# Kernel optimization log

Measured on AMD Instinct MI355X. Metric: run time of the kernel, lower is better.

Reference implementation:

```python
import jax, jax.numpy as jnp
import numpy as np
import math

B, LQ, LK = 4, 1024, 2048
QD, KD, VD = 768, 512, 512
H, NH = 1024, 16
HD = H // NH

def setup_inputs() -> dict:
    key = jax.random.key(0)
    ks = jax.random.split(key, 11)
    s = 0.02
    return {
        "query": jax.random.normal(ks[0], (B, LQ, QD), jnp.float32),
        "key": jax.random.normal(ks[1], (B, LK, KD), jnp.float32),
        "value": jax.random.normal(ks[2], (B, LK, VD), jnp.float32),
        "Wq": jax.random.normal(ks[3], (QD, H), jnp.float32) * s,
        "bq": jnp.zeros((H,), jnp.float32),
        "Wk": jax.random.normal(ks[4], (KD, H), jnp.float32) * s,
        "bk": jnp.zeros((H,), jnp.float32),
        "Wv": jax.random.normal(ks[5], (VD, H), jnp.float32) * s,
        "bv": jnp.zeros((H,), jnp.float32),
        "Wo": jax.random.normal(ks[6], (H, H), jnp.float32) * s,
        "bo": jnp.zeros((H,), jnp.float32),
    }

def reference(query, key, value, Wq, bq, Wk, bk, Wv, bv, Wo, bo):
    # project and split heads: [B, L, H] -> [B, NH, L, HD]
    def heads(x):
        b, l, _ = x.shape
        return x.reshape(b, l, NH, HD).transpose(0, 2, 1, 3)
    q = heads(query @ Wq + bq)   # [B, NH, LQ, HD]
    k = heads(key @ Wk + bk)     # [B, NH, LK, HD]
    v = heads(value @ Wv + bv)   # [B, NH, LK, HD]
    scores = jnp.einsum('bhqd,bhkd->bhqk', q, k) / math.sqrt(HD)
    weights = jax.nn.softmax(scores, axis=-1)  # dropout inactive (eval / rate used deterministically as identity)
    att = jnp.einsum('bhqk,bhkd->bhqd', weights, v)
    att = att.transpose(0, 2, 1, 3).reshape(query.shape[0], -1, H)
    out = att @ Wo + bo
    return out
```

## Files before the change

### kernel.cpp

```cpp
#include <hip/hip_runtime.h>
#include <math.h>

using bf16x8 = __attribute__((ext_vector_type(8))) short;
using f32x4  = __attribute__((ext_vector_type(4))) float;

namespace {
constexpr int kB  = 4;
constexpr int kLQ = 1024;
constexpr int kLK = 2048;
constexpr int kH  = 1024;
constexpr int kHD = 64;
}

__device__ __forceinline__ unsigned short f2bf(float x) {
  union { float f; unsigned int u; } v; v.f = x;
  unsigned int r = v.u + 0x7fffu + ((v.u >> 16) & 1u);
  return (unsigned short)(r >> 16);
}

typedef const __attribute__((address_space(1))) unsigned int guint_t;
typedef __attribute__((address_space(3))) unsigned int luint_t;
__device__ __forceinline__ void g2l16(const void* g, void* l) {
  __builtin_amdgcn_global_load_lds(
      (guint_t*)g,
      (luint_t*)(unsigned int)(unsigned long long)l,
      16, 0, 0);
}

__global__ __launch_bounds__(256) void prep_kernel(
    const float* __restrict__ q, const float* __restrict__ k,
    const float* __restrict__ v, const float* __restrict__ Wq,
    const float* __restrict__ Wk, const float* __restrict__ Wv,
    const float* __restrict__ Wo, unsigned short* __restrict__ qo,
    unsigned short* __restrict__ ko, unsigned short* __restrict__ vo,
    unsigned short* __restrict__ WqT, unsigned short* __restrict__ WkT,
    unsigned short* __restrict__ WvT, unsigned short* __restrict__ WoT)
{
  __shared__ float tile[64][65];
  const int t = threadIdx.x;
  if (blockIdx.x < 5632) {
    int c = blockIdx.x * 256 + t;
    const float* src; unsigned short* dst;
    if (c < 393216)      { src = q; dst = qo; }
    else if (c < 917504) { src = k; dst = ko; c -= 393216; }
    else                 { src = v; dst = vo; c -= 917504; }
    const int i = c * 8;
    const float4 a = *(const float4*)(src + i);
    const float4 b = *(const float4*)(src + i + 4);
    uint4 o;
    o.x = (unsigned int)f2bf(a.x) | ((unsigned int)f2bf(a.y) << 16);
    o.y = (unsigned int)f2bf(a.z) | ((unsigned int)f2bf(a.w) << 16);
    o.z = (unsigned int)f2bf(b.x) | ((unsigned int)f2bf(b.y) << 16);
    o.w = (unsigned int)f2bf(b.z) | ((unsigned int)f2bf(b.w) << 16);
    *(uint4*)(dst + i) = o;
    return;
  }
  int id = blockIdx.x - 5632;
  const float* W; unsigned short* Wt; int Kd;
  if (id < 192)      { W = Wq; Wt = WqT; Kd = 768; }
  else if (id < 320) { W = Wk; Wt = WkT; Kd = 512;  id -= 192; }
  else if (id < 448) { W = Wv; Wt = WvT; Kd = 512;  id -= 320; }
  else               { W = Wo; Wt = WoT; Kd = 1024; id -= 448; }
  const int Nd = 1024;
  const int n0 = (id & 15) * 64;
  const int k0 = (id >> 4) * 64;
  const int rr = t >> 4;
  const int c4 = t & 15;
#pragma unroll
  for (int i = 0; i < 4; ++i) {
    const int row = i * 16 + rr;
    const float4 vv = *(const float4*)(W + (size_t)(k0 + row) * Nd + n0 + c4 * 4);
    tile[row][c4*4+0] = vv.x; tile[row][c4*4+1] = vv.y;
    tile[row][c4*4+2] = vv.z; tile[row][c4*4+3] = vv.w;
  }
  __syncthreads();
#pragma unroll
  for (int i = 0; i < 4; ++i) {
    const int n = i * 16 + rr;
    ushort4 o;
    o.x = f2bf(tile[c4*4+0][n]); o.y = f2bf(tile[c4*4+1][n]);
    o.z = f2bf(tile[c4*4+2][n]); o.w = f2bf(tile[c4*4+3][n]);
    *(ushort4*)(Wt + (size_t)(n0 + n) * Kd + k0 + c4 * 4) = o;
  }
}

__device__ __forceinline__ void gemm_body(
    const unsigned short* __restrict__ A, const unsigned short* __restrict__ Bt,
    const float* __restrict__ bias, void* __restrict__ Cout,
    int N, int K, int bx, int by, int mode, char* lds)
{
  const int t    = threadIdx.x;
  const int lane = t & 63;
  const int w    = t >> 6;
  const int l15  = lane & 15;
  const int lq8  = (lane >> 4) * 8;
  const int lq4  = (lane >> 4) * 4;
  const int r0   = by * 128;
  const int c0   = bx * 128;
  const int wm   = w >> 1, wn = w & 1;

  f32x4 acc[4][4] = {};

#pragma unroll
  for (int i = 0; i < 4; ++i) {
    const int g = w * 4 + i;
    const unsigned short* src = (g < 8) ? A : Bt;
    const int rbase = (g < 8) ? (r0 + g * 16) : (c0 + (g - 8) * 16);
    g2l16(src + (size_t)(rbase + l15) * K + lq8, lds + g * 1024 + lane * 16);
  }

  int pb = 0;
  for (int k0 = 0; k0 < K; k0 += 32, pb ^= 1) {
    __syncthreads();
    char* buf = lds + pb * 16384;
    if (k0 + 32 < K) {
      char* nbuf = lds + (pb ^ 1) * 16384;
#pragma unroll
      for (int i = 0; i < 4; ++i) {
        const int g = w * 4 + i;
        const unsigned short* src = (g < 8) ? A : Bt;
        const int rbase = (g < 8) ? (r0 + g * 16) : (c0 + (g - 8) * 16);
        g2l16(src + (size_t)(rbase + l15) * K + k0 + 32 + lq8, nbuf + g * 1024 + lane * 16);
      }
    }
    bf16x8 af[4], bfr[4];
#pragma unroll
    for (int i = 0; i < 4; ++i) af[i]  = *(const bf16x8*)(buf + (wm*4 + i) * 1024 + lane * 16);
#pragma unroll
    for (int j = 0; j < 4; ++j) bfr[j] = *(const bf16x8*)(buf + 8192 + (wn*4 + j) * 1024 + lane * 16);
#pragma unroll
    for (int i = 0; i < 4; ++i)
#pragma unroll
      for (int j = 0; j < 4; ++j)
        acc[i][j] = __builtin_amdgcn_mfma_f32_16x16x32_bf16(af[i], bfr[j], acc[i][j], 0, 0, 0);
  }

#pragma unroll
  for (int j = 0; j < 4; ++j) {
    const int col = c0 + wn * 64 + j * 16 + l15;
    const float bcol = bias[col];
#pragma unroll
    for (int i = 0; i < 4; ++i) {
      const int row = r0 + wm * 64 + i * 16 + lq4;
      if (mode == 0) {
        float* out = (float*)Cout;
#pragma unroll
        for (int r = 0; r < 4; ++r) out[(size_t)(row + r) * N + col] = acc[i][j][r] + bcol;
      } else if (mode == 1) {
        unsigned short* out = (unsigned short*)Cout;
#pragma unroll
        for (int r = 0; r < 4; ++r) out[(size_t)(row + r) * N + col] = f2bf(acc[i][j][r] + bcol);
      } else {
        unsigned short* out = (unsigned short*)Cout;
        const int bb = row >> 11;
        const int lk = row & 2047;
        ushort4 o;
        o.x = f2bf(acc[i][j][0] + bcol); o.y = f2bf(acc[i][j][1] + bcol);
        o.z = f2bf(acc[i][j][2] + bcol); o.w = f2bf(acc[i][j][3] + bcol);
        *(ushort4*)(out + (size_t)(bb * kH + col) * kLK + lk) = o;
      }
    }
  }
}

__global__ __launch_bounds__(256) void qkv_gemm_kernel(
    const unsigned short* __restrict__ qA, const unsigned short* __restrict__ WqT,
    const float* __restrict__ bq, unsigned short* __restrict__ Qb,
    const unsigned short* __restrict__ kA, const unsigned short* __restrict__ WkT,
    const float* __restrict__ bk, unsigned short* __restrict__ Kb,
    const unsigned short* __restrict__ vA, const unsigned short* __restrict__ WvT,
    const float* __restrict__ bv, unsigned short* __restrict__ Vtw)
{
  __shared__ __align__(16) char lds[32768];
  int id = blockIdx.x;
  if (id < 256) {
    gemm_body(qA, WqT, bq, Qb, 1024, 768, id & 7, id >> 3, 1, lds);
  } else if (id < 768) {
    id -= 256;
    gemm_body(kA, WkT, bk, Kb, 1024, 512, id & 7, id >> 3, 1, lds);
  } else {
    id -= 768;
    gemm_body(vA, WvT, bv, Vtw, 1024, 512, id & 7, id >> 3, 2, lds);
  }
}

__global__ __launch_bounds__(256) void out_gemm_kernel(
    const unsigned short* __restrict__ A, const unsigned short* __restrict__ Bt,
    const float* __restrict__ bias, float* __restrict__ C)
{
  __shared__ __align__(16) char lds[32768];
  gemm_body(A, Bt, bias, C, 1024, 1024, blockIdx.x, blockIdx.y, 0, lds);
}

__global__ __launch_bounds__(256) void attn_mfma_kernel(
    const unsigned short* __restrict__ Q, const unsigned short* __restrict__ K,
    const unsigned short* __restrict__ Vt, unsigned short* __restrict__ O)
{
  __shared__ __align__(16) char lds[51200];
  constexpr int POFF = 32768;
  const int t    = threadIdx.x;
  const int lane = t & 63;
  const int w    = t >> 6;
  const int l15  = lane & 15;
  const int lq8  = (lane >> 4) * 8;
  const int lq4  = (lane >> 4) * 4;
  const int flat = blockIdx.x;
  const int bh   = flat & 63;
  const int qb   = flat >> 6;
  const int h    = bh & 15;
  const int b    = bh >> 4;
  const int q0   = qb * 128;
  const int hoff = h * kHD;

  bf16x8 qf[2][2];
#pragma unroll
  for (int qi = 0; qi < 2; ++qi)
#pragma unroll
    for (int kh = 0; kh < 2; ++kh)
      qf[qi][kh] = *(const bf16x8*)(Q + (size_t)(b*kLQ + q0 + w*32 + qi*16 + l15) * kH
                                      + hoff + kh*32 + lq8);

  f32x4 acc[2][4] = {};
  float lsum[2][4] = {};

#pragma unroll
  for (int i = 0; i < 4; ++i) {
    const int g = w * 4 + i;
    if (g < 8) {
      g2l16(K + (size_t)(b*kLK + (g >> 1)*16 + l15) * kH + hoff + (g & 1)*32 + lq8,
            lds + g * 1024 + lane * 16);
    } else {
      const int gg = g - 8;
      g2l16(Vt + (size_t)(b*kH + hoff + (gg >> 1)*16 + l15) * kLK + (gg & 1)*32 + lq8,
            lds + 8192 + gg * 1024 + lane * 16);
    }
  }

  int pb = 0;
  for (int kt = 0; kt < kLK / 64; ++kt, pb ^= 1) {
    __syncthreads();
    char* buf = lds + pb * 16384;
    if (kt + 1 < kLK / 64) {
      char* nbuf = lds + (pb ^ 1) * 16384;
      const int kc1 = (kt + 1) * 64;
#pragma unroll
      for (int i = 0; i < 4; ++i) {
        const int g = w * 4 + i;
        if (g < 8) {
          g2l16(K + (size_t)(b*kLK + kc1 + (g >> 1)*16 + l15) * kH + hoff + (g & 1)*32 + lq8,
                nbuf + g * 1024 + lane * 16);
        } else {
          const int gg = g - 8;
          g2l16(Vt + (size_t)(b*kH + hoff + (gg >> 1)*16 + l15) * kLK + kc1 + (gg & 1)*32 + lq8,
                nbuf + 8192 + gg * 1024 + lane * 16);
        }
      }
    }

    f32x4 s[2][4];
#pragma unroll
    for (int kcf = 0; kcf < 4; ++kcf) {
      const bf16x8 kf0 = *(const bf16x8*)(buf + (kcf*2 + 0) * 1024 + lane * 16);
      const bf16x8 kf1 = *(const bf16x8*)(buf + (kcf*2 + 1) * 1024 + lane * 16);
#pragma unroll
      for (int qi = 0; qi < 2; ++qi) {
        f32x4 z = {};
        z = __builtin_amdgcn_mfma_f32_16x16x32_bf16(qf[qi][0], kf0, z, 0, 0, 0);
        z = __builtin_amdgcn_mfma_f32_16x16x32_bf16(qf[qi][1], kf1, z, 0, 0, 0);
        s[qi][kcf] = z;
      }
    }

#pragma unroll
    for (int qi = 0; qi < 2; ++qi)
#pragma unroll
      for (int kcf = 0; kcf < 4; ++kcf)
#pragma unroll
        for (int r = 0; r < 4; ++r) {
          const float p = __builtin_amdgcn_exp2f(s[qi][kcf][r] * 0.18033688011112042f);
          lsum[qi][r] += p;
          union { float f; unsigned int u; } pu; pu.f = p;
          *(unsigned short*)(lds + POFF +
              ((w*32 + qi*16 + lq4 + r) * 72 + kcf*16 + l15) * 2) =
              (unsigned short)(pu.u >> 16);
        }

    bf16x8 pf[2][2];
#pragma unroll
    for (int qi = 0; qi < 2; ++qi)
#pragma unroll
      for (int kq = 0; kq < 2; ++kq)
        pf[qi][kq] = *(const bf16x8*)(lds + POFF +
            ((w*32 + qi*16 + l15) * 72 + kq*32 + lq8) * 2);
#pragma unroll
    for (int vd = 0; vd < 4; ++vd) {
      const bf16x8 vf0 = *(const bf16x8*)(buf + 8192 + (vd*2 + 0) * 1024 + lane * 16);
      const bf16x8 vf1 = *(const bf16x8*)(buf + 8192 + (vd*2 + 1) * 1024 + lane * 16);
#pragma unroll
      for (int qi = 0; qi < 2; ++qi) {
        acc[qi][vd] = __builtin_amdgcn_mfma_f32_16x16x32_bf16(pf[qi][0], vf0, acc[qi][vd], 0, 0, 0);
        acc[qi][vd] = __builtin_amdgcn_mfma_f32_16x16x32_bf16(pf[qi][1], vf1, acc[qi][vd], 0, 0, 0);
      }
    }
  }

#pragma unroll
  for (int qi = 0; qi < 2; ++qi)
#pragma unroll
    for (int r = 0; r < 4; ++r) {
      float v = lsum[qi][r];
      v += __shfl_xor(v, 1);
      v += __shfl_xor(v, 2);
      v += __shfl_xor(v, 4);
      v += __shfl_xor(v, 8);
      lsum[qi][r] = 1.f / v;
    }
#pragma unroll
  for (int qi = 0; qi < 2; ++qi)
#pragma unroll
    for (int vd = 0; vd < 4; ++vd)
#pragma unroll
      for (int r = 0; r < 4; ++r)
        O[(size_t)(b*kLQ + q0 + w*32 + qi*16 + lq4 + r) * kH + hoff + vd*16 + l15] =
            f2bf(acc[qi][vd][r] * lsum[qi][r]);
}

extern "C" void kernel_launch(void* const* d_in, const int* in_sizes, int n_in,
                              void* d_out, int out_size, void* d_ws, size_t ws_size,
                              hipStream_t stream) {
  (void)in_sizes; (void)n_in; (void)out_size; (void)ws_size;
  const float* query = (const float*)d_in[0];
  const float* key   = (const float*)d_in[1];
  const float* value = (const float*)d_in[2];
  const float* Wq = (const float*)d_in[3];
  const float* bq = (const float*)d_in[4];
  const float* Wk = (const float*)d_in[5];
  const float* bk = (const float*)d_in[6];
  const float* Wv = (const float*)d_in[7];
  const float* bv = (const float*)d_in[8];
  const float* Wo = (const float*)d_in[9];
  const float* bo = (const float*)d_in[10];
  float* out = (float*)d_out;

  unsigned short* ws  = (unsigned short*)d_ws;
  unsigned short* qA  = ws;
  unsigned short* kA  = qA  + 3145728;
  unsigned short* vA  = kA  + 4194304;
  unsigned short* WqT = vA  + 4194304;
  unsigned short* WkT = WqT + 786432;
  unsigned short* WvT = WkT + 524288;
  unsigned short* WoT = WvT + 524288;
  unsigned short* Qb  = WoT + 1048576;
  unsigned short* Kb  = Qb  + 4194304;
  unsigned short* Vtw = Kb  + 8388608;
  unsigned short* Ab  = Vtw + 8388608;

  dim3 blk(256);
  prep_kernel<<<6336, blk, 0, stream>>>(query, key, value, Wq, Wk, Wv, Wo,
                                        qA, kA, vA, WqT, WkT, WvT, WoT);
  qkv_gemm_kernel<<<1280, blk, 0, stream>>>(qA, WqT, bq, Qb,
                                            kA, WkT, bk, Kb,
                                            vA, WvT, bv, Vtw);
  attn_mfma_kernel<<<512, blk, 0, stream>>>(Qb, Kb, Vtw, Ab);
  out_gemm_kernel<<<dim3(8, 32), blk, 0, stream>>>(Ab, WoT, bo, out);
}
```

Before: 249.7 us.

## Enlarge QKV GEMM N-tile to 256 and attention query tile to 256

The QKV projection GEMM now computes 128x256 output tiles per block, with 8 B-fragments per wave and a larger double-buffered LDS area, which halves the grid and raises operand reuse per block. The attention kernel now handles 256 query rows per block (64 per wave). It double-buffers only K, loads V into a single buffer each step, and adds a barrier before the PV product. The output GEMM is inlined as its own 128x128 body. The aim is to cut redundant K/V and weight traffic, at the cost of fewer blocks (256 attention blocks), more registers per thread, and V loads no longer being prefetched a step ahead.

After: 260.8 us. 4.5% more time.

```diff
diff --git a/kernel.cpp b/kernel.cpp
--- a/kernel.cpp
+++ b/kernel.cpp
@@ -84,9 +84,9 @@
   }
 }
 
-__device__ __forceinline__ void gemm_body(
+__device__ __forceinline__ void gemm_body256(
     const unsigned short* __restrict__ A, const unsigned short* __restrict__ Bt,
-    const float* __restrict__ bias, void* __restrict__ Cout,
+    const float* __restrict__ bias, unsigned short* __restrict__ Cout,
     int N, int K, int bx, int by, int mode, char* lds)
 {
   const int t    = threadIdx.x;
@@ -96,14 +96,14 @@
   const int lq8  = (lane >> 4) * 8;
   const int lq4  = (lane >> 4) * 4;
   const int r0   = by * 128;
-  const int c0   = bx * 128;
+  const int c0   = bx * 256;
   const int wm   = w >> 1, wn = w & 1;
 
-  f32x4 acc[4][4] = {};
-
-#pragma unroll
-  for (int i = 0; i < 4; ++i) {
-    const int g = w * 4 + i;
+  f32x4 acc[4][8] = {};
+
+#pragma unroll
+  for (int i = 0; i < 6; ++i) {
+    const int g = w * 6 + i;
     const unsigned short* src = (g < 8) ? A : Bt;
     const int rbase = (g < 8) ? (r0 + g * 16) : (c0 + (g - 8) * 16);
     g2l16(src + (size_t)(rbase + l15) * K + lq8, lds + g * 1024 + lane * 16);
@@ -112,52 +112,46 @@
   int pb = 0;
   for (int k0 = 0; k0 < K; k0 += 32, pb ^= 1) {
     __syncthreads();
-    char* buf = lds + pb * 16384;
+    char* buf = lds + pb * 24576;
     if (k0 + 32 < K) {
-      char* nbuf = lds + (pb ^ 1) * 16384;
-#pragma unroll
-      for (int i = 0; i < 4; ++i) {
-        const int g = w * 4 + i;
+      char* nbuf = lds + (pb ^ 1) * 24576;
+#pragma unroll
+      for (int i = 0; i < 6; ++i) {
+        const int g = w * 6 + i;
         const unsigned short* src = (g < 8) ? A : Bt;
         const int rbase = (g < 8) ? (r0 + g * 16) : (c0 + (g - 8) * 16);
         g2l16(src + (size_t)(rbase + l15) * K + k0 + 32 + lq8, nbuf + g * 1024 + lane * 16);
       }
     }
-    bf16x8 af[4], bfr[4];
+    bf16x8 af[4], bfr[8];
 #pragma unroll
     for (int i = 0; i < 4; ++i) af[i]  = *(const bf16x8*)(buf + (wm*4 + i) * 1024 + lane * 16);
 #pragma unroll
-    for (int j = 0; j < 4; ++j) bfr[j] = *(const bf16x8*)(buf + 8192 + (wn*4 + j) * 1024 + lane * 16);
+    for (int j = 0; j < 8; ++j) bfr[j] = *(const bf16x8*)(buf + 8192 + (wn*8 + j) * 1024 + lane * 16);
 #pragma unroll
     for (int i = 0; i < 4; ++i)
 #pragma unroll
-      for (int j = 0; j < 4; ++j)
+      for (int j = 0; j < 8; ++j)
         acc[i][j] = __builtin_amdgcn_mfma_f32_16x16x32_bf16(af[i], bfr[j], acc[i][j], 0, 0, 0);
   }
 
 #pragma unroll
-  for (int j = 0; j < 4; ++j) {
-    const int col = c0 + wn * 64 + j * 16 + l15;
+  for (int j = 0; j < 8; ++j) {
+    const int col = c0 + wn * 128 + j * 16 + l15;
     const float bcol = bias[col];
 #pragma unroll
     for (int i = 0; i < 4; ++i) {
       const int row = r0 + wm * 64 + i * 16 + lq4;
-      if (mode == 0) {
-        float* out = (float*)Cout;
-#pragma unroll
-        for (int r = 0; r < 4; ++r) out[(size_t)(row + r) * N + col] = acc[i][j][r] + bcol;
-      } else if (mode == 1) {
-        unsigned short* out = (unsigned short*)Cout;
-#pragma unroll
-        for (int r = 0; r < 4; ++r) out[(size_t)(row + r) * N + col] = f2bf(acc[i][j][r] + bcol);
+      if (mode == 1) {
+#pragma unroll
+        for (int r = 0; r < 4; ++r) Cout[(size_t)(row + r) * N + col] = f2bf(acc[i][j][r] + bcol);
       } else {
-        unsigned short* out = (unsigned short*)Cout;
         const int bb = row >> 11;
         const int lk = row & 2047;
         ushort4 o;
         o.x = f2bf(acc[i][j][0] + bcol); o.y = f2bf(acc[i][j][1] + bcol);
         o.z = f2bf(acc[i][j][2] + bcol); o.w = f2bf(acc[i][j][3] + bcol);
-        *(ushort4*)(out + (size_t)(bb * kH + col) * kLK + lk) = o;
+        *(ushort4*)(Cout + (size_t)(bb * kH + col) * kLK + lk) = o;
       }
     }
   }
@@ -171,16 +165,16 @@
     const unsigned short* __restrict__ vA, const unsigned short* __restrict__ WvT,
     const float* __restrict__ bv, unsigned short* __restrict__ Vtw)
 {
-  __shared__ __align__(16) char lds[32768];
+  __shared__ __align__(16) char lds[49152];
   int id = blockIdx.x;
-  if (id < 256) {
-    gemm_body(qA, WqT, bq, Qb, 1024, 768, id & 7, id >> 3, 1, lds);
-  } else if (id < 768) {
-    id -= 256;
-    gemm_body(kA, WkT, bk, Kb, 1024, 512, id & 7, id >> 3, 1, lds);
+  if (id < 128) {
+    gemm_body256(qA, WqT, bq, Qb, 1024, 768, id & 3, id >> 2, 1, lds);
+  } else if (id < 384) {
+    id -= 128;
+    gemm_body256(kA, WkT, bk, Kb, 1024, 512, id & 3, id >> 2, 1, lds);
   } else {
-    id -= 768;
-    gemm_body(vA, WvT, bv, Vtw, 1024, 512, id & 7, id >> 3, 2, lds);
+    id -= 384;
+    gemm_body256(vA, WvT, bv, Vtw, 1024, 512, id & 3, id >> 2, 2, lds);
   }
 }
 
@@ -189,15 +183,71 @@
     const float* __restrict__ bias, float* __restrict__ C)
 {
   __shared__ __align__(16) char lds[32768];
-  gemm_body(A, Bt, bias, C, 1024, 1024, blockIdx.x, blockIdx.y, 0, lds);
+  const int t    = threadIdx.x;
+  const int lane = t & 63;
+  const int w    = t >> 6;
+  const int l15  = lane & 15;
+  const int lq8  = (lane >> 4) * 8;
+  const int lq4  = (lane >> 4) * 4;
+  const int r0   = blockIdx.y * 128;
+  const int c0   = blockIdx.x * 128;
+  const int wm   = w >> 1, wn = w & 1;
+  const int N = 1024, K = 1024;
+
+  f32x4 acc[4][4] = {};
+
+#pragma unroll
+  for (int i = 0; i < 4; ++i) {
+    const int g = w * 4 + i;
+    const unsigned short* src = (g < 8) ? A : Bt;
+    const int rbase = (g < 8) ? (r0 + g * 16) : (c0 + (g - 8) * 16);
+    g2l16(src + (size_t)(rbase + l15) * K + lq8, lds + g * 1024 + lane * 16);
+  }
+  int pb = 0;
+  for (int k0 = 0; k0 < K; k0 += 32, pb ^= 1) {
+    __syncthreads();
+    char* buf = lds + pb * 16384;
+    if (k0 + 32 < K) {
+      char* nbuf = lds + (pb ^ 1) * 16384;
+#pragma unroll
+      for (int i = 0; i < 4; ++i) {
+        const int g = w * 4 + i;
+        const unsigned short* src = (g < 8) ? A : Bt;
+        const int rbase = (g < 8) ? (r0 + g * 16) : (c0 + (g - 8) * 16);
+        g2l16(src + (size_t)(rbase + l15) * K + k0 + 32 + lq8, nbuf + g * 1024 + lane * 16);
+      }
+    }
+    bf16x8 af[4], bfr[4];
+#pragma unroll
+    for (int i = 0; i < 4; ++i) af[i]  = *(const bf16x8*)(buf + (wm*4 + i) * 1024 + lane * 16);
+#pragma unroll
+    for (int j = 0; j < 4; ++j) bfr[j] = *(const bf16x8*)(buf + 8192 + (wn*4 + j) * 1024 + lane * 16);
+#pragma unroll
+    for (int i = 0; i < 4; ++i)
+#pragma unroll
+      for (int j = 0; j < 4; ++j)
+        acc[i][j] = __builtin_amdgcn_mfma_f32_16x16x32_bf16(af[i], bfr[j], acc[i][j], 0, 0, 0);
+  }
+#pragma unroll
+  for (int j = 0; j < 4; ++j) {
+    const int col = c0 + wn * 64 + j * 16 + l15;
+    const float bcol = bias[col];
+#pragma unroll
+    for (int i = 0; i < 4; ++i) {
+      const int row = r0 + wm * 64 + i * 16 + lq4;
+#pragma unroll
+      for (int r = 0; r < 4; ++r) C[(size_t)(row + r) * N + col] = acc[i][j][r] + bcol;
+    }
+  }
 }
 
 __global__ __launch_bounds__(256) void attn_mfma_kernel(
     const unsigned short* __restrict__ Q, const unsigned short* __restrict__ K,
     const unsigned short* __restrict__ Vt, unsigned short* __restrict__ O)
 {
-  __shared__ __align__(16) char lds[51200];
-  constexpr int POFF = 32768;
+  __shared__ __align__(16) char lds[61440];
+  constexpr int VOFF = 16384;
+  constexpr int POFF = 24576;
   const int t    = threadIdx.x;
   const int lane = t & 63;
   const int w    = t >> 6;
@@ -209,61 +259,57 @@
   const int qb   = flat >> 6;
   const int h    = bh & 15;
   const int b    = bh >> 4;
-  const int q0   = qb * 128;
+  const int q0   = qb * 256;
   const int hoff = h * kHD;
-
-  bf16x8 qf[2][2];
-#pragma unroll
-  for (int qi = 0; qi < 2; ++qi)
+  const int qw   = w * 64;
+
+  bf16x8 qf[4][2];
+#pragma unroll
+  for (int qi = 0; qi < 4; ++qi)
 #pragma unroll
     for (int kh = 0; kh < 2; ++kh)
-      qf[qi][kh] = *(const bf16x8*)(Q + (size_t)(b*kLQ + q0 + w*32 + qi*16 + l15) * kH
+      qf[qi][kh] = *(const bf16x8*)(Q + (size_t)(b*kLQ + q0 + qw + qi*16 + l15) * kH
                                       + hoff + kh*32 + lq8);
 
-  f32x4 acc[2][4] = {};
-  float lsum[2][4] = {};
-
-#pragma unroll
-  for (int i = 0; i < 4; ++i) {
-    const int g = w * 4 + i;
-    if (g < 8) {
-      g2l16(K + (size_t)(b*kLK + (g >> 1)*16 + l15) * kH + hoff + (g & 1)*32 + lq8,
-            lds + g * 1024 + lane * 16);
-    } else {
-      const int gg = g - 8;
-      g2l16(Vt + (size_t)(b*kH + hoff + (gg >> 1)*16 + l15) * kLK + (gg & 1)*32 + lq8,
-            lds + 8192 + gg * 1024 + lane * 16);
-    }
-  }
-
-  int pb = 0;
-  for (int kt = 0; kt < kLK / 64; ++kt, pb ^= 1) {
+  f32x4 acc[4][4] = {};
+  float lsum[4][4] = {};
+
+#pragma unroll
+  for (int i = 0; i < 2; ++i) {
+    const int g = w * 2 + i;
+    g2l16(K + (size_t)(b*kLK + (g >> 1)*16 + l15) * kH + hoff + (g & 1)*32 + lq8,
+          lds + g * 1024 + lane * 16);
+  }
+
+  for (int kt = 0; kt < kLK / 64; ++kt) {
+    const int kc0 = kt * 64;
+    char* kbuf = lds + (kt & 1) * 8192;
     __syncthreads();
-    char* buf = lds + pb * 16384;
+
+#pragma unroll
+    for (int i = 0; i < 2; ++i) {
+      const int gg = w * 2 + i;
+      g2l16(Vt + (size_t)(b*kH + hoff + (gg >> 1)*16 + l15) * kLK + kc0 + (gg & 1)*32 + lq8,
+            lds + VOFF + gg * 1024 + lane * 16);
+    }
     if (kt + 1 < kLK / 64) {
-      char* nbuf = lds + (pb ^ 1) * 16384;
-      const int kc1 = (kt + 1) * 64;
-#pragma unroll
-      for (int i = 0; i < 4; ++i) {
-        const int g = w * 4 + i;
-        if (g < 8) {
-          g2l16(K + (size_t)(b*kLK + kc1 + (g >> 1)*16 + l15) * kH + hoff + (g & 1)*32 + lq8,
-                nbuf + g * 1024 + lane * 16);
-        } else {
-          const int gg = g - 8;
-          g2l16(Vt + (size_t)(b*kH + hoff + (gg >> 1)*16 + l15) * kLK + kc1 + (gg & 1)*32 + lq8,
-                nbuf + 8192 + gg * 1024 + lane * 16);
-        }
-      }
-    }
-
-    f32x4 s[2][4];
+      const int kc1 = kc0 + 64;
+      char* nkbuf = lds + ((kt + 1) & 1) * 8192;
+#pragma unroll
+      for (int i = 0; i < 2; ++i) {
+        const int g = w * 2 + i;
+        g2l16(K + (size_t)(b*kLK + kc1 + (g >> 1)*16 + l15) * kH + hoff + (g & 1)*32 + lq8,
+              nkbuf + g * 1024 + lane * 16);
+      }
+    }
+
+    f32x4 s[4][4];
 #pragma unroll
     for (int kcf = 0; kcf < 4; ++kcf) {
-      const bf16x8 kf0 = *(const bf16x8*)(buf + (kcf*2 + 0) * 1024 + lane * 16);
-      const bf16x8 kf1 = *(const bf16x8*)(buf + (kcf*2 + 1) * 1024 + lane * 16);
-#pragma unroll
-      for (int qi = 0; qi < 2; ++qi) {
+      const bf16x8 kf0 = *(const bf16x8*)(kbuf + (kcf*2 + 0) * 1024 + lane * 16);
+      const bf16x8 kf1 = *(const bf16x8*)(kbuf + (kcf*2 + 1) * 1024 + lane * 16);
+#pragma unroll
+      for (int qi = 0; qi < 4; ++qi) {
         f32x4 z = {};
         z = __builtin_amdgcn_mfma_f32_16x16x32_bf16(qf[qi][0], kf0, z, 0, 0, 0);
         z = __builtin_amdgcn_mfma_f32_16x16x32_bf16(qf[qi][1], kf1, z, 0, 0, 0);
@@ -272,7 +318,7 @@
     }
 
 #pragma unroll
-    for (int qi = 0; qi < 2; ++qi)
+    for (int qi = 0; qi < 4; ++qi)
 #pragma unroll
       for (int kcf = 0; kcf < 4; ++kcf)
 #pragma unroll
@@ -281,23 +327,25 @@
           lsum[qi][r] += p;
           union { float f; unsigned int u; } pu; pu.f = p;
           *(unsigned short*)(lds + POFF +
-              ((w*32 + qi*16 + lq4 + r) * 72 + kcf*16 + l15) * 2) =
+              ((qw + qi*16 + lq4 + r) * 72 + kcf*16 + l15) * 2) =
               (unsigned short)(pu.u >> 16);
         }
 
-    bf16x8 pf[2][2];
-#pragma unroll
-    for (int qi = 0; qi < 2; ++qi)
+    __syncthreads();
+
+    bf16x8 pf[4][2];
+#pragma unroll
+    for (int qi = 0; qi < 4; ++qi)
 #pragma unroll
       for (int kq = 0; kq < 2; ++kq)
         pf[qi][kq] = *(const bf16x8*)(lds + POFF +
-            ((w*32 + qi*16 + l15) * 72 + kq*32 + lq8) * 2);
+            ((qw + qi*16 + l15) * 72 + kq*32 + lq8) * 2);
 #pragma unroll
     for (int vd = 0; vd < 4; ++vd) {
-      const bf16x8 vf0 = *(const bf16x8*)(buf + 8192 + (vd*2 + 0) * 1024 + lane * 16);
-      const bf16x8 vf1 = *(const bf16x8*)(buf + 8192 + (vd*2 + 1) * 1024 + lane * 16);
-#pragma unroll
-      for (int qi = 0; qi < 2; ++qi) {
+      const bf16x8 vf0 = *(const bf16x8*)(lds + VOFF + (vd*2 + 0) * 1024 + lane * 16);
+      const bf16x8 vf1 = *(const bf16x8*)(lds + VOFF + (vd*2 + 1) * 1024 + lane * 16);
+#pragma unroll
+      for (int qi = 0; qi < 4; ++qi) {
         acc[qi][vd] = __builtin_amdgcn_mfma_f32_16x16x32_bf16(pf[qi][0], vf0, acc[qi][vd], 0, 0, 0);
         acc[qi][vd] = __builtin_amdgcn_mfma_f32_16x16x32_bf16(pf[qi][1], vf1, acc[qi][vd], 0, 0, 0);
       }
@@ -305,7 +353,7 @@
   }
 
 #pragma unroll
-  for (int qi = 0; qi < 2; ++qi)
+  for (int qi = 0; qi < 4; ++qi)
 #pragma unroll
     for (int r = 0; r < 4; ++r) {
       float v = lsum[qi][r];
@@ -316,12 +364,12 @@
       lsum[qi][r] = 1.f / v;
     }
 #pragma unroll
-  for (int qi = 0; qi < 2; ++qi)
+  for (int qi = 0; qi < 4; ++qi)
 #pragma unroll
     for (int vd = 0; vd < 4; ++vd)
 #pragma unroll
       for (int r = 0; r < 4; ++r)
-        O[(size_t)(b*kLQ + q0 + w*32 + qi*16 + lq4 + r) * kH + hoff + vd*16 + l15] =
+        O[(size_t)(b*kLQ + q0 + qw + qi*16 + lq4 + r) * kH + hoff + vd*16 + l15] =
             f2bf(acc[qi][vd][r] * lsum[qi][r]);
 }
 
@@ -358,9 +406,9 @@
   dim3 blk(256);
   prep_kernel<<<6336, blk, 0, stream>>>(query, key, value, Wq, Wk, Wv, Wo,
                                         qA, kA, vA, WqT, WkT, WvT, WoT);
-  qkv_gemm_kernel<<<1280, blk, 0, stream>>>(qA, WqT, bq, Qb,
-                                            kA, WkT, bk, Kb,
-                                            vA, WvT, bv, Vtw);
-  attn_mfma_kernel<<<512, blk, 0, stream>>>(Qb, Kb, Vtw, Ab);
+  qkv_gemm_kernel<<<640, blk, 0, stream>>>(qA, WqT, bq, Qb,
+                                           kA, WkT, bk, Kb,
+                                           vA, WvT, bv, Vtw);
+  attn_mfma_kernel<<<256, blk, 0, stream>>>(Qb, Kb, Vtw, Ab);
   out_gemm_kernel<<<dim3(8, 32), blk, 0, stream>>>(Ab, WoT, bo, out);
 }
```
